# Optimization experiments

Measured on AMD Instinct MI355X. Metric: run time of the kernel, lower is better.

## Reference

```python
import jax, jax.numpy as jnp
import numpy as np

N_POINTS = 8192
N_TOPICS = 64
B = 524288


def setup_inputs() -> dict:
    key = jax.random.key(0)
    k1, k2, k3, k4 = jax.random.split(key, 4)
    pij = jax.random.uniform(k1, (B,), dtype=jnp.float32, minval=1e-6, maxval=1.0)
    i = jax.random.randint(k2, (B,), 0, N_POINTS, dtype=jnp.int64)
    j = jax.random.randint(k3, (B,), 0, N_POINTS, dtype=jnp.int64)
    W = jax.random.normal(k4, (N_POINTS, N_TOPICS), dtype=jnp.float32)  # nn.Embedding weight
    return {"pij": pij, "i": i, "j": j, "W": W}


def reference(pij, i, j, W):
    # pairwise squared distances over ALL points, via the gram trick
    # (avoids materializing the [n, n, d] broadcasted tensor of the torch code)
    sq = jnp.sum(W * W, axis=1)                       # [n]
    d2 = sq[:, None] + sq[None, :] - 2.0 * (W @ W.T)  # [n, n]
    d2 = jnp.maximum(d2, 0.0)                         # numerical floor (exact math is >= 0)
    n = W.shape[0]
    # Cauchy kernel partition: sum_{k,l} 1/(1+d2) minus the n diagonal ones
    part = jnp.sum(1.0 / (1.0 + d2)) - jnp.asarray(n, d2.dtype)
    xi = W[i]                                         # [B, d]
    xj = W[j]                                         # [B, d]
    # FAITHFUL to source: (1 + diff^2).sum(1) adds 1 per dim => n_topics + ||xi-xj||^2
    num = 1.0 / jnp.sum(1.0 + (xi - xj) ** 2, axis=1)  # [B]
    qij = num / part
    loss_kld = pij * (jnp.log(pij) - jnp.log(qij))
    return jnp.sum(loss_kld)
```

## Files before the change

kernel.cpp:

```cpp
#include <hip/hip_runtime.h>
#include <math.h>

#define NPOINTS   8192
#define NDIM      64
#define TILE      128
#define NT2       64
#define NBLK      2080

#define WS_W16   0
#define WS_W8    262144
#define WS_SQ    393216
#define WS_PARTA 401408
#define WS_A1P   403488
#define WS_A3P   407584

typedef __attribute__((ext_vector_type(8))) short bf16x8;
typedef __attribute__((ext_vector_type(4))) float f32x4;
typedef __attribute__((ext_vector_type(2))) float f32x2;

__device__ inline unsigned short f2bf(float f) {
    unsigned u = __float_as_uint(f);
    u += 0x7FFFu + ((u >> 16) & 1u);
    return (unsigned short)(u >> 16);
}
template <bool HI>
__device__ inline f32x2 cvt2(unsigned dw) {
    return __builtin_amdgcn_cvt_pk_f32_fp8((int)dw, HI);
}
__device__ inline void sqacc(f32x2& s, unsigned a, unsigned b) {
    f32x2 dl = cvt2<false>(a) - cvt2<false>(b);
    f32x2 dh = cvt2<true >(a) - cvt2<true >(b);
    s += dl * dl;
    s += dh * dh;
}

__global__ __launch_bounds__(256) void prep_kernel(const float* __restrict__ W,
                                                   float* __restrict__ sq,
                                                   unsigned* __restrict__ W16,
                                                   unsigned* __restrict__ W8) {
    int t    = threadIdx.x;
    int wid  = (blockIdx.x * 256 + t) >> 6;
    int lane = t & 63;
    float v = W[wid * NDIM + lane];
    float s = v * v;
    #pragma unroll
    for (int m = 32; m >= 1; m >>= 1) s += __shfl_xor(s, m, 64);
    if (lane == 0) sq[wid] = s;
    unsigned bf   = f2bf(v);
    unsigned peer = (unsigned)__shfl_xor((int)bf, 1, 64);
    if ((lane & 1) == 0)
        W16[wid * 32 + (lane >> 1)] = (bf & 0xFFFFu) | (peer << 16);
    if (t < 64) {
        float4 x = *(const float4*)(W + blockIdx.x * 256 + t * 4);
        int lo = __builtin_amdgcn_cvt_pk_fp8_f32(x.x, x.y, 0, false);
        int dw = __builtin_amdgcn_cvt_pk_fp8_f32(x.z, x.w, lo, true);
        W8[blockIdx.x * 64 + t] = (unsigned)dw;
    }
}

__global__ __launch_bounds__(256) void pair_kernel(const unsigned* __restrict__ W8,
                                                   const float* __restrict__ pij,
                                                   const int* __restrict__ ii,
                                                   const int* __restrict__ jj,
                                                   int nb,
                                                   float* __restrict__ a1p,
                                                   float* __restrict__ a3p) {
    int t = threadIdx.x;
    int p = blockIdx.x * 256 + t;
    float a1 = 0.f, a3 = 0.f;
    if (p < nb) {
        int   i  = ii[p];
        int   j  = jj[p];
        float pv = pij[p];
        const uint4* X = (const uint4*)(W8 + i * 16);
        const uint4* Y = (const uint4*)(W8 + j * 16);
        uint4 x0 = X[0], x1 = X[1], x2 = X[2], x3 = X[3];
        uint4 y0 = Y[0], y1 = Y[1], y2 = Y[2], y3 = Y[3];
        f32x2 s2 = {0.f, 0.f};
        sqacc(s2, x0.x, y0.x); sqacc(s2, x0.y, y0.y);
        sqacc(s2, x0.z, y0.z); sqacc(s2, x0.w, y0.w);
        sqacc(s2, x1.x, y1.x); sqacc(s2, x1.y, y1.y);
        sqacc(s2, x1.z, y1.z); sqacc(s2, x1.w, y1.w);
        sqacc(s2, x2.x, y2.x); sqacc(s2, x2.y, y2.y);
        sqacc(s2, x2.z, y2.z); sqacc(s2, x2.w, y2.w);
        sqacc(s2, x3.x, y3.x); sqacc(s2, x3.y, y3.y);
        sqacc(s2, x3.z, y3.z); sqacc(s2, x3.w, y3.w);
        float v = s2.x + s2.y;
        a1 = pv * __logf(pv * ((float)NDIM + v));
        a3 = pv;
    }
    #pragma unroll
    for (int m = 32; m >= 1; m >>= 1) {
        a1 += __shfl_xor(a1, m, 64);
        a3 += __shfl_xor(a3, m, 64);
    }
    __shared__ float red[8];
    if ((t & 63) == 0) { red[t >> 6] = a1; red[4 + (t >> 6)] = a3; }
    __syncthreads();
    if (t == 0) {
        a1p[blockIdx.x] = red[0] + red[1] + red[2] + red[3];
        a3p[blockIdx.x] = red[4] + red[5] + red[6] + red[7];
    }
}

__global__ __launch_bounds__(256) void pairwise_kernel(const unsigned* __restrict__ W16,
                                                       const float* __restrict__ sq,
                                                       float* __restrict__ partA) {
    int z = blockIdx.x;
    int t = threadIdx.x, w = t >> 6, lane = t & 63;
    int by = (int)((129.0 - sqrt(16641.0 - 8.0 * (double)z)) * 0.5);
    while (by * NT2 - by * (by - 1) / 2 > z) --by;
    while ((by + 1) * NT2 - (by + 1) * by / 2 <= z) ++by;
    int bx = by + (z - (by * NT2 - by * (by - 1) / 2));

    int wm = w >> 1, wn = w & 1, quad = lane >> 4, l15 = lane & 15;
    int a0 = by * TILE, b0 = bx * TILE;

    float4 base1[4];
    float  sqb[4];
    {
        int arow = a0 + wm * 64 + quad * 4;
        #pragma unroll
        for (int tm = 0; tm < 4; ++tm) {
            float4 v = *(const float4*)(sq + arow + tm * 16);
            base1[tm] = (float4){1.0f + v.x, 1.0f + v.y, 1.0f + v.z, 1.0f + v.w};
        }
        int bcol = b0 + wn * 64 + l15;
        #pragma unroll
        for (int tn = 0; tn < 4; ++tn) sqb[tn] = sq[bcol + tn * 16];
    }

    f32x4 acc[4][4];
    #pragma unroll
    for (int i = 0; i < 4; ++i)
        #pragma unroll
        for (int j = 0; j < 4; ++j) acc[i][j] = (f32x4){0.f, 0.f, 0.f, 0.f};

    const unsigned* Arow = W16 + (a0 + wm * 64 + l15) * 32;
    const unsigned* Brow = W16 + (b0 + wn * 64 + l15) * 32;
    #pragma unroll
    for (int h = 0; h < 2; ++h) {
        bf16x8 af[4], bfr[4];
        #pragma unroll
        for (int tm = 0; tm < 4; ++tm)
            af[tm] = *(const bf16x8*)(Arow + tm * 16 * 32 + h * 16 + quad * 4);
        #pragma unroll
        for (int tn = 0; tn < 4; ++tn)
            bfr[tn] = *(const bf16x8*)(Brow + tn * 16 * 32 + h * 16 + quad * 4);
        #pragma unroll
        for (int tm = 0; tm < 4; ++tm)
            #pragma unroll
            for (int tn = 0; tn < 4; ++tn)
                acc[tm][tn] = __builtin_amdgcn_mfma_f32_16x16x32_bf16(af[tm], bfr[tn],
                                                                      acc[tm][tn], 0, 0, 0);
    }

    float ssum = 0.f;
    if (bx > by) {
        #pragma unroll
        for (int tn = 0; tn < 4; ++tn) {
            float c0 = sqb[tn];
            #pragma unroll
            for (int tm = 0; tm < 4; ++tm) {
                ssum += __builtin_amdgcn_rcpf(fmaf(acc[tm][tn][0], -2.0f, base1[tm].x + c0));
                ssum += __builtin_amdgcn_rcpf(fmaf(acc[tm][tn][1], -2.0f, base1[tm].y + c0));
                ssum += __builtin_amdgcn_rcpf(fmaf(acc[tm][tn][2], -2.0f, base1[tm].z + c0));
                ssum += __builtin_amdgcn_rcpf(fmaf(acc[tm][tn][3], -2.0f, base1[tm].w + c0));
            }
        }
    } else {
        int quad4 = quad * 4;
        #pragma unroll
        for (int tn = 0; tn < 4; ++tn) {
            int cl = wn * 64 + tn * 16 + l15;
            float c0 = sqb[tn];
            float b4[4];
            #pragma unroll
            for (int tm = 0; tm < 4; ++tm) {
                b4[0] = base1[tm].x; b4[1] = base1[tm].y;
                b4[2] = base1[tm].z; b4[3] = base1[tm].w;
                #pragma unroll
                for (int r = 0; r < 4; ++r) {
                    int rl = wm * 64 + tm * 16 + quad4 + r;
                    float inv = __builtin_amdgcn_rcpf(fmaf(acc[tm][tn][r], -2.0f, b4[r] + c0));
                    ssum += (cl > rl) ? inv : 0.f;
                }
            }
        }
    }
    #pragma unroll
    for (int m = 32; m >= 1; m >>= 1) ssum += __shfl_xor(ssum, m, 64);
    __shared__ float wsum[4];
    if (lane == 0) wsum[w] = ssum;
    __syncthreads();
    if (t == 0) partA[z] = wsum[0] + wsum[1] + wsum[2] + wsum[3];
}

__global__ __launch_bounds__(256) void final_kernel(const float* __restrict__ partA,
                                                    const float* __restrict__ a1p,
                                                    const float* __restrict__ a3p,
                                                    int npb,
                                                    float* __restrict__ out) {
    __shared__ double r1[256], r2[256], r3[256];
    int t = threadIdx.x;
    double dpart = 0.0, d1 = 0.0, d3 = 0.0;
    for (int k = t; k < NBLK; k += 256) dpart += (double)partA[k];
    for (int k = t; k < npb; k += 256) { d1 += (double)a1p[k]; d3 += (double)a3p[k]; }
    r1[t] = dpart; r2[t] = d1; r3[t] = d3;
    __syncthreads();
    for (int s = 128; s >= 1; s >>= 1) {
        if (t < s) { r1[t] += r1[t + s]; r2[t] += r2[t + s]; r3[t] += r3[t + s]; }
        __syncthreads();
    }
    if (t == 0) {
        double part = 2.0 * r1[0];
        out[0] = (float)(r2[0] + r3[0] * log(part));
    }
}

extern "C" void kernel_launch(void* const* d_in, const int* in_sizes, int n_in,
                              void* d_out, int out_size, void* d_ws, size_t ws_size,
                              hipStream_t stream) {
    const float* pij = (const float*)d_in[0];
    const int*   ii  = (const int*)d_in[1];
    const int*   jj  = (const int*)d_in[2];
    const float* W   = (const float*)d_in[3];
    float* out = (float*)d_out;
    float* ws  = (float*)d_ws;

    unsigned* W16   = (unsigned*)ws + WS_W16;
    unsigned* W8    = (unsigned*)ws + WS_W8;
    float*    sqv   = ws + WS_SQ;
    float*    partA = ws + WS_PARTA;
    float*    a1p   = ws + WS_A1P;
    float*    a3p   = ws + WS_A3P;

    int nb  = in_sizes[0];
    int npb = (nb + 255) / 256;

    prep_kernel<<<NPOINTS / 4, 256, 0, stream>>>(W, sqv, W16, W8);
    pair_kernel<<<npb, 256, 0, stream>>>(W8, pij, ii, jj, nb, a1p, a3p);
    pairwise_kernel<<<NBLK, 256, 0, stream>>>(W16, sqv, partA);
    final_kernel<<<1, 256, 0, stream>>>(partA, a1p, a3p, npb, out);
}
```

Baseline: 102.3 us.

## Store bf16 W in MFMA fragment-major layout for coalesced pairwise loads

The prep kernel now writes the bf16 copy of W in a layout grouped by 16-row blocks and K-halves, so each lane's 16-byte MFMA operand sits contiguously at lane*4. Pairwise loads then become fully coalesced 1 KB wave reads instead of strided row reads. Prep is also restructured around 16 rows per block with float4 loads, and the triangular tile index uses a float sqrt instead of a double one. The float sqrt leans on the existing correction loops to stay exact.

New measurement: 91.37 us, median of 2. 1.12x faster.

```diff
diff --git a/kernel.cpp b/kernel.cpp
--- a/kernel.cpp
+++ b/kernel.cpp
@@ -6,6 +6,7 @@
 #define TILE      128
 #define NT2       64
 #define NBLK      2080
+#define NGRP      512
 
 #define WS_W16   0
 #define WS_W8    262144
@@ -18,10 +19,11 @@
 typedef __attribute__((ext_vector_type(4))) float f32x4;
 typedef __attribute__((ext_vector_type(2))) float f32x2;
 
-__device__ inline unsigned short f2bf(float f) {
-    unsigned u = __float_as_uint(f);
-    u += 0x7FFFu + ((u >> 16) & 1u);
-    return (unsigned short)(u >> 16);
+__device__ inline unsigned f2bf_pk(float lo, float hi) {
+    unsigned ul = __float_as_uint(lo), uh = __float_as_uint(hi);
+    ul += 0x7FFFu + ((ul >> 16) & 1u);
+    uh += 0x7FFFu + ((uh >> 16) & 1u);
+    return (ul >> 16) | (uh & 0xFFFF0000u);
 }
 template <bool HI>
 __device__ inline f32x2 cvt2(unsigned dw) {
@@ -36,25 +38,36 @@
 
 __global__ __launch_bounds__(256) void prep_kernel(const float* __restrict__ W,
                                                    float* __restrict__ sq,
-                                                   unsigned* __restrict__ W16,
+                                                   unsigned* __restrict__ W16f,
                                                    unsigned* __restrict__ W8) {
-    int t    = threadIdx.x;
-    int wid  = (blockIdx.x * 256 + t) >> 6;
-    int lane = t & 63;
-    float v = W[wid * NDIM + lane];
-    float s = v * v;
-    #pragma unroll
-    for (int m = 32; m >= 1; m >>= 1) s += __shfl_xor(s, m, 64);
-    if (lane == 0) sq[wid] = s;
-    unsigned bf   = f2bf(v);
-    unsigned peer = (unsigned)__shfl_xor((int)bf, 1, 64);
-    if ((lane & 1) == 0)
-        W16[wid * 32 + (lane >> 1)] = (bf & 0xFFFFu) | (peer << 16);
-    if (t < 64) {
-        float4 x = *(const float4*)(W + blockIdx.x * 256 + t * 4);
+    int g = blockIdx.x;
+    int t = threadIdx.x;
+
+    {
+        int h = t >> 7, L = (t >> 1) & 63, dp = t & 1;
+        int row = g * 16 + (L & 15), quad = L >> 4;
+        float4 v = *(const float4*)(W + row * NDIM + h * 32 + quad * 8 + dp * 4);
+        uint2 o;
+        o.x = f2bf_pk(v.x, v.y);
+        o.y = f2bf_pk(v.z, v.w);
+        *(uint2*)(W16f + ((g * 2 + h) * 256 + L * 4 + dp * 2)) = o;
+    }
+    {
+        int r = t >> 4, s = t & 15;
+        float4 v = *(const float4*)(W + (g * 16 + r) * NDIM + s * 4);
+        float p = v.x * v.x + v.y * v.y + v.z * v.z + v.w * v.w;
+        p += __shfl_xor(p, 1, 64);
+        p += __shfl_xor(p, 2, 64);
+        p += __shfl_xor(p, 4, 64);
+        p += __shfl_xor(p, 8, 64);
+        if (s == 0) sq[g * 16 + r] = p;
+    }
+    {
+        int r = g * 16 + (t >> 4), d = t & 15;
+        float4 x = *(const float4*)(W + r * NDIM + d * 4);
         int lo = __builtin_amdgcn_cvt_pk_fp8_f32(x.x, x.y, 0, false);
         int dw = __builtin_amdgcn_cvt_pk_fp8_f32(x.z, x.w, lo, true);
-        W8[blockIdx.x * 64 + t] = (unsigned)dw;
+        W8[r * 16 + d] = (unsigned)dw;
     }
 }
 
@@ -103,12 +116,12 @@
     }
 }
 
-__global__ __launch_bounds__(256) void pairwise_kernel(const unsigned* __restrict__ W16,
+__global__ __launch_bounds__(256) void pairwise_kernel(const unsigned* __restrict__ W16f,
                                                        const float* __restrict__ sq,
                                                        float* __restrict__ partA) {
     int z = blockIdx.x;
     int t = threadIdx.x, w = t >> 6, lane = t & 63;
-    int by = (int)((129.0 - sqrt(16641.0 - 8.0 * (double)z)) * 0.5);
+    int by = (int)((129.0f - sqrtf((float)(16641 - 8 * z))) * 0.5f);
     while (by * NT2 - by * (by - 1) / 2 > z) --by;
     while ((by + 1) * NT2 - (by + 1) * by / 2 <= z) ++by;
     int bx = by + (z - (by * NT2 - by * (by - 1) / 2));
@@ -136,17 +149,17 @@
         #pragma unroll
         for (int j = 0; j < 4; ++j) acc[i][j] = (f32x4){0.f, 0.f, 0.f, 0.f};
 
-    const unsigned* Arow = W16 + (a0 + wm * 64 + l15) * 32;
-    const unsigned* Brow = W16 + (b0 + wn * 64 + l15) * 32;
+    int gA = (a0 >> 4) + wm * 4;
+    int gB = (b0 >> 4) + wn * 4;
     #pragma unroll
     for (int h = 0; h < 2; ++h) {
         bf16x8 af[4], bfr[4];
         #pragma unroll
         for (int tm = 0; tm < 4; ++tm)
-            af[tm] = *(const bf16x8*)(Arow + tm * 16 * 32 + h * 16 + quad * 4);
+            af[tm] = *(const bf16x8*)(W16f + (((gA + tm) * 2 + h) * 256 + lane * 4));
         #pragma unroll
         for (int tn = 0; tn < 4; ++tn)
-            bfr[tn] = *(const bf16x8*)(Brow + tn * 16 * 32 + h * 16 + quad * 4);
+            bfr[tn] = *(const bf16x8*)(W16f + (((gB + tn) * 2 + h) * 256 + lane * 4));
         #pragma unroll
         for (int tm = 0; tm < 4; ++tm)
             #pragma unroll
@@ -228,7 +241,7 @@
     float* out = (float*)d_out;
     float* ws  = (float*)d_ws;
 
-    unsigned* W16   = (unsigned*)ws + WS_W16;
+    unsigned* W16f  = (unsigned*)ws + WS_W16;
     unsigned* W8    = (unsigned*)ws + WS_W8;
     float*    sqv   = ws + WS_SQ;
     float*    partA = ws + WS_PARTA;
@@ -238,8 +251,8 @@
     int nb  = in_sizes[0];
     int npb = (nb + 255) / 256;
 
-    prep_kernel<<<NPOINTS / 4, 256, 0, stream>>>(W, sqv, W16, W8);
+    prep_kernel<<<NGRP, 256, 0, stream>>>(W, sqv, W16f, W8);
     pair_kernel<<<npb, 256, 0, stream>>>(W8, pij, ii, jj, nb, a1p, a3p);
-    pairwise_kernel<<<NBLK, 256, 0, stream>>>(W16, sqv, partA);
+    pairwise_kernel<<<NBLK, 256, 0, stream>>>(W16f, sqv, partA);
     final_kernel<<<1, 256, 0, stream>>>(partA, a1p, a3p, npb, out);
 }
```
